# Kernel optimization log

Hardware: AMD Instinct MI355X
Metric: run time of the kernel (lower is better)

## Reference

```python
import jax, jax.numpy as jnp
import numpy as np

B, H, W, Q, E, M, K, WIN = 4, 192, 192, 160, 96, 96, 4, 7
NO_ELECTRON_WEIGHT = 0.1


def _bce_logits(x, z):
    # binary_cross_entropy_with_logits, elementwise: softplus(x) - x*z
    return jnp.logaddexp(0.0, x) - x * z


def setup_inputs() -> dict:
    key = jax.random.key(0)
    ks = jax.random.split(key, 11)
    is_electron_logit = jax.random.normal(ks[0], (B * Q,), jnp.float32)
    true_segmap = jax.random.uniform(ks[1], (B, H, W, E), jnp.float32)
    binary_mask_logits = jax.random.normal(ks[2], (B, H, W, Q), jnp.float32)
    portion_logits = jax.random.normal(ks[3], (B, H, W, Q), jnp.float32)
    # keep incidence points away from borders so the 7x7 window stays in-bounds
    incidence_points = jax.random.uniform(ks[4], (B, E, 2), jnp.float32) * (H - 8) + 4.0
    positions = jax.random.uniform(ks[5], (B, Q, 2), jnp.float32) * H
    a = jax.random.normal(ks[6], (B, Q, 3), jnp.float32)
    l00 = jax.nn.softplus(a[..., 0]) + 0.1
    l11 = jax.nn.softplus(a[..., 2]) + 0.1
    l10 = 0.5 * a[..., 1]
    zero = jnp.zeros_like(l00)
    chol = jnp.stack([jnp.stack([l00, zero], -1), jnp.stack([l10, l11], -1)], -2)  # [B,Q,2,2] lower-tri
    occupancy_logits = jax.random.normal(ks[7], (B, H, W, K), jnp.float32)
    occupancy_true = jax.random.randint(ks[8], (B, H, W), 0, K, jnp.int32)
    qkeys = jax.random.split(ks[9], B)
    matched_q = jnp.stack([jax.random.permutation(k, Q)[:M] for k in qkeys]).astype(jnp.int32)
    ekeys = jax.random.split(ks[10], B)
    matched_e = jnp.stack([jax.random.permutation(k, E) for k in ekeys]).astype(jnp.int32)
    return dict(is_electron_logit=is_electron_logit, true_segmap=true_segmap,
                binary_mask_logits=binary_mask_logits, portion_logits=portion_logits,
                incidence_points=incidence_points, positions=positions, chol=chol,
                occupancy_logits=occupancy_logits, occupancy_true=occupancy_true,
                matched_q=matched_q, matched_e=matched_e)


def reference(is_electron_logit, true_segmap, binary_mask_logits, portion_logits,
              incidence_points, positions, chol, occupancy_logits, occupancy_true,
              matched_q, matched_e):
    # ---- class loss (weighted BCE over flat per-query logits) ----
    labels = jnp.zeros((B * Q,), is_electron_logit.dtype)
    glob = (jnp.arange(B)[:, None] * Q + matched_q).reshape(-1)
    labels = labels.at[glob].set(1.0)
    weights = jnp.where(labels > 0, 1.0, NO_ELECTRON_WEIGHT).astype(is_electron_logit.dtype)
    class_loss = jnp.mean(weights * _bce_logits(is_electron_logit, labels))

    # ---- reorder segmentation maps to matched order (_reorder_segmentation_map) ----
    true_r = jnp.take_along_axis(true_segmap, matched_e[:, None, None, :], axis=3)        # [B,H,W,M]
    bin_r = jnp.take_along_axis(binary_mask_logits, matched_q[:, None, None, :], axis=3)  # [B,H,W,M]
    por_r = jnp.take_along_axis(portion_logits, matched_q[:, None, None, :], axis=3)      # [B,H,W,M]

    # ---- mask BCE on 7x7 windows around floor(matched incidence point) ----
    pts_r = jnp.take_along_axis(incidence_points, matched_e[..., None], axis=1)  # [B,M,2]
    pix = jnp.floor(pts_r).astype(jnp.int32)
    half = WIN // 2
    dr = jnp.arange(-half, half + 1)
    rows = pix[..., 0][:, :, None, None] + dr[None, None, :, None]  # [B,M,7,1]
    cols = pix[..., 1][:, :, None, None] + dr[None, None, None, :]  # [B,M,1,7]
    bi = jnp.arange(B)[:, None, None, None]
    mi = jnp.arange(M)[None, :, None, None]
    tv = true_r[bi, rows, cols, mi]  # [B,M,7,7]
    lg = bin_r[bi, rows, cols, mi]
    bce_loss = jnp.mean(_bce_logits(lg, tv))

    # ---- dice loss (softmax over matched-electron dim) ----
    portion = jax.nn.softmax(por_r, axis=-1)
    num = jnp.sum(2.0 * true_r * portion, axis=(1, 2, 3))
    den = jnp.sum(true_r + portion, axis=(1, 2, 3))
    dice_loss = jnp.mean(1.0 - (num + 1.0) / (den + 1.0))

    # ---- distance NLL (2D MVN with lower-tri scale) ----
    centers_r = jnp.take_along_axis(positions, matched_q[..., None], axis=1)       # [B,M,2]
    chol_r = jnp.take_along_axis(chol, matched_q[..., None, None], axis=1)         # [B,M,2,2]
    d = pts_r - centers_r
    z0 = d[..., 0] / chol_r[..., 0, 0]
    z1 = (d[..., 1] - chol_r[..., 1, 0] * z0) / chol_r[..., 1, 1]
    nll = 0.5 * (z0 * z0 + z1 * z1) + jnp.log(2.0 * jnp.pi) \
          + jnp.log(chol_r[..., 0, 0]) + jnp.log(chol_r[..., 1, 1])
    nll = jnp.where(jnp.isinf(nll), 1e7, nll)
    nll_loss = jnp.mean(nll)

    # ---- occupancy loss (per-pixel electron-count cross-entropy) ----
    logp = jax.nn.log_softmax(occupancy_logits, axis=-1)
    occ_loss = -jnp.mean(jnp.take_along_axis(logp, occupancy_true[..., None], axis=-1))

    # loss_weights all 1.0 (defaults); dot(weights, terms)
    return class_loss + bce_loss + dice_loss + nll_loss + occ_loss
```

## Files before the change

### kernel.cpp

```cpp
#include <hip/hip_runtime.h>
#include <math.h>

#define B_ 4
#define H_ 192
#define W_ 192
#define Q_ 160
#define E_ 96
#define M_ 96
#define HW_ (H_ * W_)
#define NPIX_ (B_ * HW_)
#define TPIX 16
#define NTILE_B 2304
#define TILES_PER_BLK 9
#define NDICE 1024
#define NSMALL 962
#define NBUCKET 64
#define WS_NUM0 4
#define WS_TS0  260
#define WS_TOTAL 516

template <int CTRL, int RMASK>
__device__ inline float dpp_add_step(float x) {
    int v = __builtin_amdgcn_update_dpp(0, __float_as_int(x), CTRL, RMASK, 0xF, false);
    return x + __int_as_float(v);
}
__device__ inline float wave_sum63(float x) {
    x = dpp_add_step<0x111, 0xF>(x);
    x = dpp_add_step<0x112, 0xF>(x);
    x = dpp_add_step<0x114, 0xF>(x);
    x = dpp_add_step<0x118, 0xF>(x);
    x = dpp_add_step<0x142, 0xA>(x);
    x = dpp_add_step<0x143, 0xC>(x);
    return x;
}

__device__ inline float waveSumAll(float v) {
    for (int m = 32; m > 0; m >>= 1) v += __shfl_xor(v, m, 64);
    return v;
}

__device__ inline float softplusf(float x) {
    return fmaxf(x, 0.f) + log1pf(__expf(-fabsf(x)));
}

#define POR_BYTES (TPIX * Q_ * 4)
#define TRU_BYTES (TPIX * E_ * 4)
#define TILE_BYTES (POR_BYTES + TRU_BYTES)
#define POR_F (TPIX * Q_)

__global__ __launch_bounds__(256) void fused_kernel(
    const float* __restrict__ logit,
    const float* __restrict__ trueseg,
    const float* __restrict__ binlog,
    const float* __restrict__ por,
    const float* __restrict__ inc,
    const float* __restrict__ pos,
    const float* __restrict__ chol,
    const float* __restrict__ occlog,
    const int* __restrict__ occtrue,
    const int* __restrict__ mqall,
    const int* __restrict__ meall,
    float* __restrict__ ws)
{
    __shared__ float4 tilebuf[TILE_BYTES / 16];
    __shared__ float red[256];
    __shared__ float sA[4], sT[4];
    __shared__ float lab[B_ * Q_];
    const int tid  = threadIdx.x;
    const int lane = tid & 63;
    const int wid  = tid >> 6;
    const int blk  = blockIdx.x;

    if (blk < NDICE) {
        const int b = blk >> 8;
        const int slot = blk & 255;
        const bool hi = lane < 32;
        const int* mq = mqall + b * M_;
        const int* me = meall + b * M_;
        const int mqa = mq[lane];
        const int mea = me[lane];
        int mqb = 0, meb = 0;
        if (hi) { mqb = mq[64 + lane]; meb = me[64 + lane]; }
        const char* porb = (const char*)(por + (size_t)b * HW_ * Q_);
        const char* trb  = (const char*)(trueseg + (size_t)b * HW_ * E_);

        float4 pf[4];
        auto load_tile = [&](int t) {
            const int p0 = (slot + t * 256) * TPIX;
            const char* gp = porb + (size_t)p0 * (Q_ * 4);
            const char* gt = trb  + (size_t)p0 * (E_ * 4);
            #pragma unroll
            for (int i = 0; i < 4; ++i) {
                int off = tid * 16 + i * 4096;
                pf[i] = (off < POR_BYTES)
                        ? *(const float4*)(gp + off)
                        : *(const float4*)(gt + (off - POR_BYTES));
            }
        };
        auto store_tile = [&]() {
            #pragma unroll
            for (int i = 0; i < 4; ++i) tilebuf[tid + i * 256] = pf[i];
        };

        const float* pl = (const float*)tilebuf;
        const float* tl = (const float*)tilebuf + POR_F;
        float an = 0.f;
        float at = 0.f;

        load_tile(0);
        for (int t = 0; t < TILES_PER_BLK; ++t) {
            store_tile();
            __syncthreads();
            if (t + 1 < TILES_PER_BLK) load_tile(t + 1);
            #pragma unroll
            for (int k = 0; k < 4; ++k) {
                const int pix = wid * 4 + k;
                float p0v = pl[pix * Q_ + mqa];
                float t0  = tl[pix * E_ + mea];
                float e1 = 0.f, se1 = 0.f, t1 = 0.f;
                if (hi) {
                    float p1 = pl[pix * Q_ + mqb];
                    t1 = tl[pix * E_ + meb];
                    e1 = __expf(p1);
                    se1 = t1 * e1;
                }
                float e0 = __expf(p0v);
                float s  = wave_sum63(e0 + e1);
                float se = wave_sum63(t0 * e0 + se1);
                an += __fdividef(se, s);
                at += t0 + t1;
            }
            __syncthreads();
        }
        float atr = wave_sum63(at);
        if (lane == 63) { sA[wid] = an; sT[wid] = atr; }
        __syncthreads();
        if (tid == 0) {
            float num = sA[0] + sA[1] + sA[2] + sA[3];
            float ts  = sT[0] + sT[1] + sT[2] + sT[3];
            int bucket = blk & (NBUCKET - 1);
            atomicAdd(&ws[WS_NUM0 + bucket * 4 + b], 2.f * num);
            atomicAdd(&ws[WS_TS0  + bucket * 4 + b], ts);
        }
    } else {
        const int s = blk - NDICE;
        float acc = 0.f;
        if (s == 0) {
            for (int i = tid; i < B_ * Q_; i += 256) lab[i] = 0.f;
            __syncthreads();
            for (int i = tid; i < B_ * M_; i += 256) {
                int b = i / M_;
                lab[b * Q_ + mqall[i]] = 1.f;
            }
            __syncthreads();
            for (int i = tid; i < B_ * Q_; i += 256) {
                float x = logit[i];
                float z = lab[i];
                float w = z > 0.f ? 1.f : 0.1f;
                acc += w * (softplusf(x) - x * z);
            }
            red[tid] = acc; __syncthreads();
            for (int st = 128; st > 0; st >>= 1) { if (tid < st) red[tid] += red[tid + st]; __syncthreads(); }
            if (tid == 0) ws[0] = red[0];
        } else if (s == 1) {
            for (int i = tid; i < B_ * M_; i += 256) {
                int b = i / M_;
                int qi = mqall[i];
                int ei = meall[i];
                float px = inc[(b * E_ + ei) * 2 + 0];
                float py = inc[(b * E_ + ei) * 2 + 1];
                float cx = pos[(b * Q_ + qi) * 2 + 0];
                float cy = pos[(b * Q_ + qi) * 2 + 1];
                const float* ch = chol + (size_t)(b * Q_ + qi) * 4;
                float l00 = ch[0], l10 = ch[2], l11 = ch[3];
                float d0 = px - cx, d1 = py - cy;
                float z0 = d0 / l00;
                float z1 = (d1 - l10 * z0) / l11;
                float nll = 0.5f * (z0 * z0 + z1 * z1) + 1.837877066409345f
                            + logf(l00) + logf(l11);
                if (isinf(nll)) nll = 1e7f;
                acc += nll;
            }
            red[tid] = acc; __syncthreads();
            for (int st = 128; st > 0; st >>= 1) { if (tid < st) red[tid] += red[tid + st]; __syncthreads(); }
            if (tid == 0) ws[2] = red[0];
        } else if (s < 386) {
            int idx = s - 2;
            int b = idx / M_;
            int ei = meall[idx];
            int qi = mqall[idx];
            float px = inc[(b * E_ + ei) * 2 + 0];
            float py = inc[(b * E_ + ei) * 2 + 1];
            int r0 = (int)floorf(px) - 3;
            int c0 = (int)floorf(py) - 3;
            if (tid < 49) {
                int rr = r0 + tid / 7;
                int cc = c0 + tid % 7;
                size_t pix = ((size_t)b * H_ + rr) * W_ + cc;
                float tv = trueseg[pix * E_ + ei];
                float lg = binlog[pix * Q_ + qi];
                acc = softplusf(lg) - lg * tv;
            }
            red[tid] = acc; __syncthreads();
            for (int st = 128; st > 0; st >>= 1) { if (tid < st) red[tid] += red[tid + st]; __syncthreads(); }
            if (tid == 0) atomicAdd(&ws[1], red[0]);
        } else {
            int p = (s - 386) * 256 + tid;
            if (p < NPIX_) {
                float4 v = *(const float4*)(occlog + (size_t)p * 4);
                int lb = occtrue[p];
                float m = fmaxf(fmaxf(v.x, v.y), fmaxf(v.z, v.w));
                float lse = m + __logf(__expf(v.x - m) + __expf(v.y - m) +
                                       __expf(v.z - m) + __expf(v.w - m));
                float xs = lb == 0 ? v.x : (lb == 1 ? v.y : (lb == 2 ? v.z : v.w));
                acc = lse - xs;
            }
            red[tid] = acc; __syncthreads();
            for (int st = 128; st > 0; st >>= 1) { if (tid < st) red[tid] += red[tid + st]; __syncthreads(); }
            if (tid == 0) atomicAdd(&ws[3], red[0]);
        }
    }
}

__global__ __launch_bounds__(64) void final_kernel(const float* __restrict__ ws,
                                                   float* __restrict__ out)
{
    const int lane = threadIdx.x;
    float n[B_], t[B_];
    for (int b = 0; b < B_; ++b) {
        n[b] = waveSumAll(ws[WS_NUM0 + lane * 4 + b]);
        t[b] = waveSumAll(ws[WS_TS0  + lane * 4 + b]);
    }
    if (lane == 0) {
        float class_l = ws[0] * (1.f / (B_ * Q_));
        float bce_l   = ws[1] * (1.f / (B_ * M_ * 49));
        float nll_l   = ws[2] * (1.f / (B_ * M_));
        float occ_l   = ws[3] * (1.f / NPIX_);
        float dice = 0.f;
        for (int b = 0; b < B_; ++b)
            dice += 1.f - (n[b] + 1.f) / (t[b] + (float)HW_ + 1.f);
        dice *= (1.f / B_);
        out[0] = class_l + bce_l + nll_l + occ_l + dice;
    }
}

extern "C" void kernel_launch(void* const* d_in, const int* in_sizes, int n_in,
                              void* d_out, int out_size, void* d_ws, size_t ws_size,
                              hipStream_t stream) {
    const float* logit   = (const float*)d_in[0];
    const float* trueseg = (const float*)d_in[1];
    const float* binlog  = (const float*)d_in[2];
    const float* por     = (const float*)d_in[3];
    const float* inc     = (const float*)d_in[4];
    const float* pos     = (const float*)d_in[5];
    const float* chol    = (const float*)d_in[6];
    const float* occlog  = (const float*)d_in[7];
    const int*   occtrue = (const int*)d_in[8];
    const int*   mq      = (const int*)d_in[9];
    const int*   me      = (const int*)d_in[10];
    float* out = (float*)d_out;
    float* ws  = (float*)d_ws;

    (void)hipMemsetAsync(d_ws, 0, WS_TOTAL * sizeof(float), stream);

    hipLaunchKernelGGL(fused_kernel, dim3(NDICE + NSMALL), dim3(256), 0, stream,
                       logit, trueseg, binlog, por, inc, pos, chol, occlog, occtrue,
                       mq, me, ws);
    hipLaunchKernelGGL(final_kernel, dim3(1), dim3(64), 0, stream, ws, out);
}
```

Measured before the change: 259.7 us.

## Stage dice tiles directly into LDS with double-buffered global_load_lds

Replaces the register-staged tile loads (global load into float4 registers, then store to shared memory) with direct global-to-LDS DMA loads into two alternating LDS buffers. This removes the register round-trip and the trailing barrier in each tile iteration, so the fetch of the next tile can overlap the softmax and reduction work on the current one. The LDS tile footprint doubles, which may lower occupancy. To offset part of that, the scratch arrays used by the small-loss blocks are aliased onto the tile buffer. Correctness depends on the compiler inserting the right memory-count waits before the loaded data is read.

```diff
diff --git a/kernel.cpp b/kernel.cpp
--- a/kernel.cpp
+++ b/kernel.cpp
@@ -10,7 +10,6 @@
 #define HW_ (H_ * W_)
 #define NPIX_ (B_ * HW_)
 #define TPIX 16
-#define NTILE_B 2304
 #define TILES_PER_BLK 9
 #define NDICE 1024
 #define NSMALL 962
@@ -19,12 +18,23 @@
 #define WS_TS0  260
 #define WS_TOTAL 516
 
+#define POR_BYTES (TPIX * Q_ * 4)
+#define TRU_BYTES (TPIX * E_ * 4)
+#define TILE_BYTES (POR_BYTES + TRU_BYTES)
+#define POR_F (TPIX * Q_)
+
+__device__ __forceinline__ void stage16(const void* g, void* l) {
+    __builtin_amdgcn_global_load_lds(
+        (const __attribute__((address_space(1))) void*)g,
+        (__attribute__((address_space(3))) void*)l, 16, 0, 0);
+}
+
 template <int CTRL, int RMASK>
-__device__ inline float dpp_add_step(float x) {
+__device__ __forceinline__ float dpp_add_step(float x) {
     int v = __builtin_amdgcn_update_dpp(0, __float_as_int(x), CTRL, RMASK, 0xF, false);
     return x + __int_as_float(v);
 }
-__device__ inline float wave_sum63(float x) {
+__device__ __forceinline__ float wave_sum63(float x) {
     x = dpp_add_step<0x111, 0xF>(x);
     x = dpp_add_step<0x112, 0xF>(x);
     x = dpp_add_step<0x114, 0xF>(x);
@@ -34,19 +44,14 @@
     return x;
 }
 
-__device__ inline float waveSumAll(float v) {
+__device__ __forceinline__ float waveSumAll(float v) {
     for (int m = 32; m > 0; m >>= 1) v += __shfl_xor(v, m, 64);
     return v;
 }
 
-__device__ inline float softplusf(float x) {
+__device__ __forceinline__ float softplusf(float x) {
     return fmaxf(x, 0.f) + log1pf(__expf(-fabsf(x)));
 }
-
-#define POR_BYTES (TPIX * Q_ * 4)
-#define TRU_BYTES (TPIX * E_ * 4)
-#define TILE_BYTES (POR_BYTES + TRU_BYTES)
-#define POR_F (TPIX * Q_)
 
 __global__ __launch_bounds__(256) void fused_kernel(
     const float* __restrict__ logit,
@@ -62,10 +67,8 @@
     const int* __restrict__ meall,
     float* __restrict__ ws)
 {
-    __shared__ float4 tilebuf[TILE_BYTES / 16];
-    __shared__ float red[256];
+    __shared__ float tilebuf[2 * TILE_BYTES / 4];
     __shared__ float sA[4], sT[4];
-    __shared__ float lab[B_ * Q_];
     const int tid  = threadIdx.x;
     const int lane = tid & 63;
     const int wid  = tid >> 6;
@@ -84,34 +87,40 @@
         const char* porb = (const char*)(por + (size_t)b * HW_ * Q_);
         const char* trb  = (const char*)(trueseg + (size_t)b * HW_ * E_);
 
-        float4 pf[4];
-        auto load_tile = [&](int t) {
-            const int p0 = (slot + t * 256) * TPIX;
+        float an = 0.f;
+        float at = 0.f;
+
+        {
+            const int p0 = slot * TPIX;
             const char* gp = porb + (size_t)p0 * (Q_ * 4);
             const char* gt = trb  + (size_t)p0 * (E_ * 4);
             #pragma unroll
             for (int i = 0; i < 4; ++i) {
-                int off = tid * 16 + i * 4096;
-                pf[i] = (off < POR_BYTES)
-                        ? *(const float4*)(gp + off)
-                        : *(const float4*)(gt + (off - POR_BYTES));
-            }
-        };
-        auto store_tile = [&]() {
-            #pragma unroll
-            for (int i = 0; i < 4; ++i) tilebuf[tid + i * 256] = pf[i];
-        };
-
-        const float* pl = (const float*)tilebuf;
-        const float* tl = (const float*)tilebuf + POR_F;
-        float an = 0.f;
-        float at = 0.f;
-
-        load_tile(0);
+                const int off = i * 4096 + wid * 1024;
+                const char* src = (off < POR_BYTES) ? (gp + off)
+                                                    : (gt + (off - POR_BYTES));
+                stage16(src + lane * 16, (char*)tilebuf + off);
+            }
+        }
+
+        int bufsel = 0;
         for (int t = 0; t < TILES_PER_BLK; ++t) {
-            store_tile();
             __syncthreads();
-            if (t + 1 < TILES_PER_BLK) load_tile(t + 1);
+            if (t + 1 < TILES_PER_BLK) {
+                const int p0 = (slot + (t + 1) * 256) * TPIX;
+                const char* gp = porb + (size_t)p0 * (Q_ * 4);
+                const char* gt = trb  + (size_t)p0 * (E_ * 4);
+                const int nb = bufsel ^ 1;
+                #pragma unroll
+                for (int i = 0; i < 4; ++i) {
+                    const int off = i * 4096 + wid * 1024;
+                    const char* src = (off < POR_BYTES) ? (gp + off)
+                                                        : (gt + (off - POR_BYTES));
+                    stage16(src + lane * 16, (char*)tilebuf + nb * TILE_BYTES + off);
+                }
+            }
+            const float* pl = tilebuf + bufsel * (TILE_BYTES / 4);
+            const float* tl = pl + POR_F;
             #pragma unroll
             for (int k = 0; k < 4; ++k) {
                 const int pix = wid * 4 + k;
@@ -130,7 +139,7 @@
                 an += __fdividef(se, s);
                 at += t0 + t1;
             }
-            __syncthreads();
+            bufsel ^= 1;
         }
         float atr = wave_sum63(at);
         if (lane == 63) { sA[wid] = an; sT[wid] = atr; }
@@ -143,6 +152,8 @@
             atomicAdd(&ws[WS_TS0  + bucket * 4 + b], ts);
         }
     } else {
+        float* red = tilebuf;
+        float* lab = tilebuf + 256;
         const int s = blk - NDICE;
         float acc = 0.f;
         if (s == 0) {
```

Measured after the change: 243.0 us. 6.4% less time.
